# Performance work log

Hardware: AMD Instinct MI355X
Metric: run time of the kernel (lower is better)

Reference implementation:

```python
import jax, jax.numpy as jnp
import numpy as np

EPS = 1e-6

def _layernorm(x, gamma, beta):
    mu = jnp.mean(x, axis=-1, keepdims=True)
    var = jnp.mean(jnp.square(x - mu), axis=-1, keepdims=True)
    return (x - mu) * jax.lax.rsqrt(var + EPS) * gamma + beta


def setup_inputs() -> dict:
    key = jax.random.key(0)
    ks = jax.random.split(key, 8)
    B, N, C, F = 2, 2048, 1024, 4096
    s = 0.02
    return {
        "x": jax.random.normal(ks[0], (B, N, C), jnp.float32),
        "Wq": jax.random.normal(ks[1], (C, C), jnp.float32) * s,
        "Wk": jax.random.normal(ks[2], (C, C), jnp.float32) * s,
        "Wv": jax.random.normal(ks[3], (C, C), jnp.float32) * s,
        "Wp": jax.random.normal(ks[4], (C, C), jnp.float32) * s,
        "bp": jnp.zeros((C,), jnp.float32),
        "W1": jax.random.normal(ks[5], (C, F), jnp.float32) * s,
        "b1": jnp.zeros((F,), jnp.float32),
        "W2": jax.random.normal(ks[6], (F, C), jnp.float32) * s,
        "b2": jnp.zeros((C,), jnp.float32),
        "gamma1": jnp.ones((C,), jnp.float32),
        "beta1": jnp.zeros((C,), jnp.float32),
        "gamma2": jnp.ones((C,), jnp.float32),
        "beta2": jnp.zeros((C,), jnp.float32),
    }


def reference(x, Wq, Wk, Wv, Wp, bp, W1, b1, W2, b2, gamma1, beta1, gamma2, beta2):
    B, N, C = x.shape
    H = 16
    D = C // H
    scale = D ** -0.5

    xn = _layernorm(x, gamma1, beta1)
    # QKV projections (no bias); q pre-scaled by head_dim**-0.5 as in source
    q = (xn @ Wq * scale).reshape(B, N, H, D).transpose(0, 2, 1, 3)  # bhnd
    k = (xn @ Wk).reshape(B, N, H, D).transpose(0, 2, 1, 3)
    v = (xn @ Wv).reshape(B, N, H, D).transpose(0, 2, 1, 3)

    attn = jax.nn.softmax(jnp.einsum("bhnd,bhmd->bhnm", q, k), axis=-1)
    y = jnp.einsum("bhnm,bhmd->bhnd", attn, v)
    y = y.transpose(0, 2, 1, 3).reshape(B, N, C)
    x = x + (y @ Wp + bp)

    xn2 = _layernorm(x, gamma2, beta2)
    h = jax.nn.gelu(xn2 @ W1 + b1, approximate=False)  # keras 'gelu' is exact
    x = x + (h @ W2 + b2)
    return x
```

## Files before the change

kernel.cpp:

```cpp
#include <hip/hip_runtime.h>
#include <math.h>

#define BN  4096
#define SEQ 2048
#define CH  1024
#define FF  4096
#define NH  16
#define HD  64

typedef short bf16x8 __attribute__((ext_vector_type(8)));
typedef float f32x4  __attribute__((ext_vector_type(4)));

#define MFMA16(a,b,c) __builtin_amdgcn_mfma_f32_16x16x32_bf16(a,b,c,0,0,0)

__device__ __forceinline__ unsigned short f2b(float f){
  unsigned u = __float_as_uint(f);
  u += 0x7fffu + ((u>>16)&1u);
  return (unsigned short)(u>>16);
}

__device__ __forceinline__ unsigned pk2(float a, float b){
  return __builtin_amdgcn_perm(__float_as_uint(b), __float_as_uint(a), 0x07060302u);
}

#if __has_builtin(__builtin_amdgcn_exp2f)
__device__ __forceinline__ float fexp2(float x){ return __builtin_amdgcn_exp2f(x); }
#else
__device__ __forceinline__ float fexp2(float x){
  float r; asm("v_exp_f32 %0, %1" : "=v"(r) : "v"(x)); return r;
}
#endif

__device__ __forceinline__ void gl2lds16(const void* g, void* l){
  __builtin_amdgcn_global_load_lds(
      (__attribute__((address_space(1))) void*)g,
      (__attribute__((address_space(3))) void*)l, 16, 0, 0);
}

__device__ __forceinline__ unsigned xcd_chunk(unsigned id, unsigned nwg){
  const unsigned cpx = nwg >> 3;
  return (id & 7u)*cpx + (id >> 3);
}

__global__ __launch_bounds__(256) void transpose_cvt(const float* __restrict__ in,
    unsigned short* __restrict__ out, int R, int S, float scale)
{
  __shared__ float tile[64][65];
  const int tid = threadIdx.x;
  const int tx = tid & 63, ty = tid >> 6;
  const int s0 = blockIdx.x * 64, r0 = blockIdx.y * 64;
  #pragma unroll
  for (int j = 0; j < 16; j++){
    int r = ty + j*4;
    tile[r][tx] = in[(size_t)(r0 + r)*S + s0 + tx];
  }
  __syncthreads();
  #pragma unroll
  for (int j = 0; j < 16; j++){
    int s = ty + j*4;
    out[(size_t)(s0 + s)*R + r0 + tx] = f2b(tile[tx][s] * scale);
  }
}

__global__ __launch_bounds__(256) void ln_kernel(const float* __restrict__ x,
    const float* __restrict__ gamma, const float* __restrict__ beta,
    unsigned short* __restrict__ out)
{
  const int row = blockIdx.x, tid = threadIdx.x;
  const float4 xv = ((const float4*)(x + (size_t)row*CH))[tid];
  float s  = xv.x + xv.y + xv.z + xv.w;
  float ss = xv.x*xv.x + xv.y*xv.y + xv.z*xv.z + xv.w*xv.w;
  #pragma unroll
  for (int off = 1; off < 64; off <<= 1){
    s  += __shfl_xor(s,  off, 64);
    ss += __shfl_xor(ss, off, 64);
  }
  __shared__ float red[8];
  const int w = tid >> 6;
  if ((tid & 63) == 0){ red[w] = s; red[4+w] = ss; }
  __syncthreads();
  s  = red[0]+red[1]+red[2]+red[3];
  ss = red[4]+red[5]+red[6]+red[7];
  const float mu   = s * (1.f/CH);
  const float rstd = rsqrtf(ss*(1.f/CH) - mu*mu + 1e-6f);
  const float4 g = ((const float4*)gamma)[tid];
  const float4 b = ((const float4*)beta )[tid];
  ushort4 o;
  o.x = f2b((xv.x-mu)*rstd*g.x + b.x);
  o.y = f2b((xv.y-mu)*rstd*g.y + b.y);
  o.z = f2b((xv.z-mu)*rstd*g.z + b.z);
  o.w = f2b((xv.w-mu)*rstd*g.w + b.w);
  ((ushort4*)(out + (size_t)row*CH))[tid] = o;
}

template<int BIAS,int GELU,int RES,int OMODE>
__global__ __launch_bounds__(256,4) void gemm128(const unsigned short* __restrict__ A,
    const unsigned short* __restrict__ Bt, const float* __restrict__ bias,
    const float* __restrict__ resid, float* __restrict__ outF,
    unsigned short* __restrict__ outB, unsigned short* __restrict__ outK,
    unsigned short* __restrict__ outV, int M, int Nn, int K)
{
  __shared__ __align__(16) char lds[32768];
  const int tid = threadIdx.x;
  const int w = tid >> 6, lane = tid & 63;
  const int quad = lane >> 4, l16 = lane & 15;
  const unsigned Wid = xcd_chunk(blockIdx.y*gridDim.x + blockIdx.x,
                                 gridDim.x*gridDim.y);
  const int bx = Wid % gridDim.x, by = Wid / gridDim.x;
  const int m0 = by*128, n0 = bx*128;
  const int wm = (w >> 1)*64, wn = (w & 1)*64;
  f32x4 acc[4][4] = {};
  const int nt = K >> 5;

  const int ci0 = w*2, ci1 = w*2 + 1;
  const int ra0 = ci0*16 + (lane >> 2);
  const int ra1 = ra0 + 16;
  const int ga0 = (lane & 3) ^ ((ra0 >> 1) & 3);
  const int ga1 = (lane & 3) ^ ((ra1 >> 1) & 3);
  const unsigned short* aS0 = A  + (size_t)(m0 + ra0)*K + ga0*8;
  const unsigned short* aS1 = A  + (size_t)(m0 + ra1)*K + ga1*8;
  const unsigned short* bS0 = Bt + (size_t)(n0 + ra0)*K + ga0*8;
  const unsigned short* bS1 = Bt + (size_t)(n0 + ra1)*K + ga1*8;

  auto STAGE = [&](int buf){
    char* Ad = lds + buf*8192;
    char* Bd = lds + 16384 + buf*8192;
    gl2lds16(aS0, Ad + ci0*1024);
    gl2lds16(aS1, Ad + ci1*1024);
    gl2lds16(bS0, Bd + ci0*1024);
    gl2lds16(bS1, Bd + ci1*1024);
    aS0 += 32; aS1 += 32; bS0 += 32; bS1 += 32;
  };

  STAGE(0);
  __syncthreads();
  for (int t = 0; t < nt; t++){
    const int cur = t & 1;
    if (t + 1 < nt) STAGE(cur ^ 1);
    const unsigned short* Ac = (const unsigned short*)(lds + cur*8192);
    const unsigned short* Bc = (const unsigned short*)(lds + 16384 + cur*8192);
    bf16x8 af[4], bfr[4];
    #pragma unroll
    for (int mi = 0; mi < 4; mi++){
      const int r = wm + mi*16 + l16;
      af[mi] = *(const bf16x8*)(Ac + r*32 + ((quad ^ ((r >> 1) & 3))*8));
    }
    #pragma unroll
    for (int nj = 0; nj < 4; nj++){
      const int r = wn + nj*16 + l16;
      bfr[nj] = *(const bf16x8*)(Bc + r*32 + ((quad ^ ((r >> 1) & 3))*8));
    }
    #pragma unroll
    for (int mi = 0; mi < 4; mi++)
      #pragma unroll
      for (int nj = 0; nj < 4; nj++)
        acc[mi][nj] = MFMA16(af[mi], bfr[nj], acc[mi][nj]);
    __syncthreads();
  }

  const int colb = n0 + wn;
  const int row0 = m0 + wm;
  if (OMODE == 1 || OMODE == 3){
    unsigned short* scr = (unsigned short*)lds + w*4096;
    const int cg = (OMODE == 3) ? (colb >> 10) : 0;
    #pragma unroll
    for (int nj = 0; nj < 4; nj++){
      const int col = colb + nj*16 + l16;
      const float bv = BIAS ? bias[col] : 0.f;
      #pragma unroll
      for (int mi = 0; mi < 4; mi++){
        #pragma unroll
        for (int r = 0; r < 4; r++){
          const int rl = mi*16 + quad*4 + r;
          float v = acc[mi][nj][r] + bv;
          if (GELU) v = 0.5f*v*(1.f + erff(v*0.70710678118654752f));
          if (RES)  v += resid[(size_t)(row0 + rl)*Nn + col];
          const unsigned short b16 = f2b(v);
          if (OMODE == 3 && cg == 2){
            const int d = nj*16 + l16;
            scr[d*64 + (((rl & 15) << 2) | (rl >> 4))] = b16;
          } else {
            scr[rl*64 + nj*16 + l16] = b16;
          }
        }
      }
    }
    const int sl = (lane & 7)*8;
    #pragma unroll
    for (int j = 0; j < 8; j++){
      const int rr = j*8 + (lane >> 3);
      const bf16x8 vv = *(const bf16x8*)(scr + rr*64 + sl);
      if (OMODE == 1){
        *(bf16x8*)(outB + (size_t)(row0 + rr)*Nn + colb + sl) = vv;
      } else {
        if (cg == 0)
          *(bf16x8*)(outB + (size_t)(row0 + rr)*CH + (colb & (CH-1)) + sl) = vv;
        else if (cg == 1)
          *(bf16x8*)(outK + (size_t)(row0 + rr)*CH + (colb & (CH-1)) + sl) = vv;
        else {
          const int bb = row0 >> 11;
          const int hh = (colb & (CH-1)) >> 6;
          *(bf16x8*)(outV + ((size_t)((bb*NH + hh)*HD) + rr)*SEQ
                          + (row0 & (SEQ-1)) + sl) = vv;
        }
      }
    }
    return;
  }
  #pragma unroll
  for (int nj = 0; nj < 4; nj++){
    const int col = colb + nj*16 + l16;
    const float bv = BIAS ? bias[col] : 0.f;
    #pragma unroll
    for (int mi = 0; mi < 4; mi++){
      #pragma unroll
      for (int r = 0; r < 4; r++){
        const int row = row0 + mi*16 + quad*4 + r;
        float v = acc[mi][nj][r] + bv;
        if (GELU) v = 0.5f*v*(1.f + erff(v*0.70710678118654752f));
        if (RES)  v += resid[(size_t)row*Nn + col];
        outF[(size_t)row*Nn + col] = v;
      }
    }
  }
}

template<int BNT,int BIAS,int GELU,int RES,int OMODE,int SPLITK>
__global__ __launch_bounds__(256,2) void gemm_bt(const unsigned short* __restrict__ A,
    const unsigned short* __restrict__ Bt, const float* __restrict__ bias,
    const float* __restrict__ resid, float* __restrict__ outF,
    unsigned short* __restrict__ outB, unsigned short* __restrict__ outK,
    unsigned short* __restrict__ outV, int M, int Nn, int K)
{
  constexpr int MI  = (BNT==128) ? 4 : 2;
  constexpr int BCH = (BNT==128) ? 4 : 2;
  constexpr int ABYTES = 128*64*2;
  constexpr int BBYTES = BNT*64*2;
  __shared__ __align__(16) char lds[2*ABYTES + 2*BBYTES];
  const int tid = threadIdx.x;
  const int w = tid >> 6, lane = tid & 63;
  const int quad = lane >> 4, l16 = lane & 15;
  const unsigned Wid = xcd_chunk(blockIdx.y*gridDim.x + blockIdx.x,
                                 gridDim.x*gridDim.y);
  const int bx = Wid % gridDim.x, by = Wid / gridDim.x;
  const int m0 = by*128, n0 = bx*BNT;
  const int wm = (BNT==128) ? (w >> 1)*64 : w*32;
  const int wn = (BNT==128) ? (w & 1)*64 : 0;
  const int srow = lane >> 3, sslot = lane & 7;
  f32x4 acc[MI][4] = {};
  const int kseg = SPLITK > 1 ? K / SPLITK : K;
  const int kBeg = SPLITK > 1 ? blockIdx.z * kseg : 0;
  const int nsteps = kseg >> 6;

  auto STAGE = [&](int buf, int k0){
    char* Ad = lds + buf*ABYTES;
    char* Bd = lds + 2*ABYTES + buf*BBYTES;
    #pragma unroll
    for (int i = 0; i < 4; i++){
      const int rb = (w*4 + i)*8;
      const int r = rb + srow;
      const int c = sslot ^ (r & 7);
      gl2lds16(A + (size_t)(m0 + r)*K + k0 + c*8, Ad + rb*128);
    }
    #pragma unroll
    for (int i = 0; i < BCH; i++){
      const int rb = (w*BCH + i)*8;
      const int r = rb + srow;
      const int c = sslot ^ (r & 7);
      gl2lds16(Bt + (size_t)(n0 + r)*K + k0 + c*8, Bd + rb*128);
    }
  };

  STAGE(0, kBeg);
  __syncthreads();
  for (int t = 0; t < nsteps; t++){
    const int cur = t & 1;
    if (t + 1 < nsteps) STAGE(cur ^ 1, kBeg + (t+1)*64);
    const unsigned short* Ac = (const unsigned short*)(lds + cur*ABYTES);
    const unsigned short* Bc = (const unsigned short*)(lds + 2*ABYTES + cur*BBYTES);
    #pragma unroll
    for (int kc = 0; kc < 2; kc++){
      bf16x8 af[MI], bfr[4];
      #pragma unroll
      for (int mi = 0; mi < MI; mi++){
        const int r = wm + mi*16 + l16;
        af[mi] = *(const bf16x8*)(Ac + r*64 + (((kc*4 + quad) ^ (r & 7))*8));
      }
      #pragma unroll
      for (int nj = 0; nj < 4; nj++){
        const int r = wn + nj*16 + l16;
        bfr[nj] = *(const bf16x8*)(Bc + r*64 + (((kc*4 + quad) ^ (r & 7))*8));
      }
      #pragma unroll
      for (int mi = 0; mi < MI; mi++)
        #pragma unroll
        for (int nj = 0; nj < 4; nj++)
          acc[mi][nj] = MFMA16(af[mi], bfr[nj], acc[mi][nj]);
    }
    __syncthreads();
  }

  #pragma unroll
  for (int nj = 0; nj < 4; nj++){
    const int col = n0 + wn + nj*16 + l16;
    const float bv = BIAS ? bias[col] : 0.f;
    #pragma unroll
    for (int mi = 0; mi < MI; mi++){
      #pragma unroll
      for (int r = 0; r < 4; r++){
        const int row = m0 + wm + mi*16 + quad*4 + r;
        float v = acc[mi][nj][r];
        if (SPLITK > 1){
          if (blockIdx.z == 0){
            if (BIAS) v += bias[col];
            if (RES)  v += resid[(size_t)row*Nn + col];
          }
          atomicAdd(&outF[(size_t)row*Nn + col], v);
          continue;
        }
        v += bv;
        if (GELU) v = 0.5f*v*(1.f + erff(v*0.70710678118654752f));
        if (RES)  v += resid[(size_t)row*Nn + col];
        if (OMODE == 0) outF[(size_t)row*Nn + col] = v;
        else outB[(size_t)row*Nn + col] = f2b(v);
      }
    }
  }
}

__global__ __launch_bounds__(256,2) void attn_kernel(const unsigned short* __restrict__ q,
    const unsigned short* __restrict__ k, const unsigned short* __restrict__ vt,
    unsigned short* __restrict__ y)
{
  __shared__ __align__(16) unsigned short Kl[2][64*64];
  __shared__ __align__(16) unsigned short Vl[2][64*64];
  __shared__ __align__(16) unsigned short Pp[4][64*68];
  const int tid = threadIdx.x;
  const int w = tid >> 6, lane = tid & 63;
  const int wq = w & 1, wk = w >> 1;
  const int quad = lane >> 4, l16 = lane & 15;
  const unsigned Wid = xcd_chunk(blockIdx.y*gridDim.x + blockIdx.x,
                                 gridDim.x*gridDim.y);
  const int qt = Wid & 15, bh = Wid >> 4;
  const int b = bh >> 4, h = bh & 15;
  const size_t tb  = ((size_t)b*SEQ)*CH + h*HD;
  const size_t vb_ = (size_t)bh*HD*SEQ;
  const int qr0 = qt*128 + wq*64;

  bf16x8 qf[4][2];
  #pragma unroll
  for (int mi = 0; mi < 4; mi++)
    #pragma unroll
    for (int kc = 0; kc < 2; kc++)
      qf[mi][kc] = *(const bf16x8*)(q + tb + (size_t)(qr0 + mi*16 + l16)*CH + kc*32 + quad*8);

  float sacc[4][4];
  f32x4 o[4][4] = {};
  #pragma unroll
  for (int mi = 0; mi < 4; mi++)
    #pragma unroll
    for (int r = 0; r < 4; r++) sacc[mi][r] = 0.f;

  for (int t = 0; t < 16; t++){
    const int kv0 = wk*1024 + t*64;
    __syncthreads();
    #pragma unroll
    for (int i = 0; i < 8; i++){
      const int r = i*8 + (lane >> 3);
      const int c = (lane & 7) ^ (r & 7);
      if (wq == 0)
        gl2lds16(k  + tb  + (size_t)(kv0 + r)*CH + c*8, (char*)&Kl[wk][0] + i*1024);
      else
        gl2lds16(vt + vb_ + (size_t)r*SEQ + kv0 + c*8, (char*)&Vl[wk][0] + i*1024);
    }
    __syncthreads();

    f32x4 s[4][4] = {};
    #pragma unroll
    for (int kc = 0; kc < 2; kc++){
      #pragma unroll
      for (int nj = 0; nj < 4; nj++){
        bf16x8 kf = *(const bf16x8*)(&Kl[wk][0] + (nj*16 + l16)*64 + (((kc*4 + quad) ^ (l16 & 7))*8));
        #pragma unroll
        for (int mi = 0; mi < 4; mi++)
          s[mi][nj] = MFMA16(qf[mi][kc], kf, s[mi][nj]);
      }
    }
    #pragma unroll
    for (int mi = 0; mi < 4; mi++){
      #pragma unroll
      for (int r = 0; r < 4; r++){
        const float p0 = fexp2(s[mi][0][r]);
        const float p1 = fexp2(s[mi][1][r]);
        const float p2 = fexp2(s[mi][2][r]);
        const float p3 = fexp2(s[mi][3][r]);
        sacc[mi][r] += (p0 + p1) + (p2 + p3);
        uint2 pk;
        pk.x = pk2(p0, p1);
        pk.y = pk2(p2, p3);
        const int prow = mi*16 + quad*4 + r;
        *(uint2*)(&Pp[w][prow*68 + l16*4]) = pk;
      }
    }
    #pragma unroll
    for (int kc = 0; kc < 2; kc++){
      bf16x8 pa[4];
      #pragma unroll
      for (int mi = 0; mi < 4; mi++)
        pa[mi] = *(const bf16x8*)(&Pp[w][(mi*16 + l16)*68 + kc*32 + quad*8]);
      #pragma unroll
      for (int nd = 0; nd < 4; nd++){
        bf16x8 vf = *(const bf16x8*)(&Vl[wk][0] + (nd*16 + l16)*64 + (((kc*4 + quad) ^ (l16 & 7))*8));
        #pragma unroll
        for (int mi = 0; mi < 4; mi++)
          o[mi][nd] = MFMA16(pa[mi], vf, o[mi][nd]);
      }
    }
  }

  __syncthreads();
  float* ob = wq ? (float*)&Vl[0][0] : (float*)&Kl[0][0];
  float* sb = (float*)&Pp[2 + wq][0];
  if (wk == 1){
    #pragma unroll
    for (int mi = 0; mi < 4; mi++)
      #pragma unroll
      for (int nd = 0; nd < 4; nd++)
        #pragma unroll
        for (int r = 0; r < 4; r++){
          const int idx = (mi*4 + nd)*4 + r;
          ob[lane*64 + ((idx + lane) & 63)] = o[mi][nd][r];
        }
    #pragma unroll
    for (int mi = 0; mi < 4; mi++)
      #pragma unroll
      for (int r = 0; r < 4; r++)
        sb[lane*16 + ((mi*4 + r + lane) & 15)] = sacc[mi][r];
  }
  __syncthreads();
  if (wk == 0){
    #pragma unroll
    for (int mi = 0; mi < 4; mi++)
      #pragma unroll
      for (int nd = 0; nd < 4; nd++)
        #pragma unroll
        for (int r = 0; r < 4; r++){
          const int idx = (mi*4 + nd)*4 + r;
          o[mi][nd][r] += ob[lane*64 + ((idx + lane) & 63)];
        }
    #pragma unroll
    for (int mi = 0; mi < 4; mi++){
      #pragma unroll
      for (int r = 0; r < 4; r++){
        float sum = sacc[mi][r] + sb[lane*16 + ((mi*4 + r + lane) & 15)];
        #pragma unroll
        for (int off = 1; off < 16; off <<= 1) sum += __shfl_xor(sum, off, 64);
        const float inv = 1.f / sum;
        const int qr = qr0 + mi*16 + quad*4 + r;
        #pragma unroll
        for (int nd = 0; nd < 4; nd++)
          y[tb + (size_t)qr*CH + nd*16 + l16] = f2b(o[mi][nd][r]*inv);
      }
    }
  }
}

extern "C" void kernel_launch(void* const* d_in, const int* in_sizes, int n_in,
                              void* d_out, int out_size, void* d_ws, size_t ws_size,
                              hipStream_t stream)
{
  (void)in_sizes; (void)n_in; (void)out_size; (void)ws_size;
  const float* x   = (const float*)d_in[0];
  const float* Wq  = (const float*)d_in[1];
  const float* Wk  = (const float*)d_in[2];
  const float* Wv  = (const float*)d_in[3];
  const float* Wp  = (const float*)d_in[4];
  const float* bp  = (const float*)d_in[5];
  const float* W1  = (const float*)d_in[6];
  const float* b1  = (const float*)d_in[7];
  const float* W2  = (const float*)d_in[8];
  const float* b2  = (const float*)d_in[9];
  const float* g1  = (const float*)d_in[10];
  const float* be1 = (const float*)d_in[11];
  const float* g2  = (const float*)d_in[12];
  const float* be2 = (const float*)d_in[13];
  float* out = (float*)d_out;
  char* ws = (char*)d_ws;
  const size_t MB = 1024*1024;
  unsigned short* wq_t = (unsigned short*)(ws +  0*MB);
  unsigned short* wk_t = (unsigned short*)(ws +  2*MB);
  unsigned short* wv_t = (unsigned short*)(ws +  4*MB);
  unsigned short* wp_t = (unsigned short*)(ws +  6*MB);
  unsigned short* w1_t = (unsigned short*)(ws +  8*MB);
  unsigned short* w2_t = (unsigned short*)(ws + 16*MB);
  unsigned short* xn   = (unsigned short*)(ws + 24*MB);
  unsigned short* qb   = (unsigned short*)(ws + 32*MB);
  unsigned short* kb   = (unsigned short*)(ws + 40*MB);
  unsigned short* vtb  = (unsigned short*)(ws + 48*MB);
  unsigned short* yb   = (unsigned short*)(ws + 56*MB);
  float*          x2   = (float*)         (ws + 64*MB);
  unsigned short* xn2  = (unsigned short*)(ws + 80*MB);
  unsigned short* hb   = (unsigned short*)(ws + 88*MB);

  transpose_cvt<<<dim3(16,16),256,0,stream>>>(Wq, wq_t, CH, CH, 0.18033688011112042f);
  transpose_cvt<<<dim3(16,16),256,0,stream>>>(Wk, wk_t, CH, CH, 1.f);
  transpose_cvt<<<dim3(16,16),256,0,stream>>>(Wv, wv_t, CH, CH, 1.f);
  transpose_cvt<<<dim3(16,16),256,0,stream>>>(Wp, wp_t, CH, CH, 1.f);
  transpose_cvt<<<dim3(64,16),256,0,stream>>>(W1, w1_t, CH, FF, 1.f);
  transpose_cvt<<<dim3(16,64),256,0,stream>>>(W2, w2_t, FF, CH, 1.f);

  ln_kernel<<<BN,256,0,stream>>>(x, g1, be1, xn);
  gemm128<0,0,0,3><<<dim3(24,32),256,0,stream>>>(xn, wq_t, nullptr, nullptr,
      nullptr, qb, kb, vtb, BN, 3072, CH);
  attn_kernel<<<dim3(16,32),256,0,stream>>>(qb, kb, vtb, yb);
  gemm_bt<64,1,0,1,0,0><<<dim3(16,32),256,0,stream>>>(yb, wp_t, bp, x, x2,
      nullptr, nullptr, nullptr, BN, CH, CH);
  ln_kernel<<<BN,256,0,stream>>>(x2, g2, be2, xn2);
  gemm128<1,1,0,1><<<dim3(32,32),256,0,stream>>>(xn2, w1_t, b1, nullptr, nullptr,
      hb, nullptr, nullptr, BN, FF, CH);
  gemm_bt<64,1,0,1,0,0><<<dim3(16,32),256,0,stream>>>(hb, w2_t, b2, x2, out,
      nullptr, nullptr, nullptr, BN, CH, FF);
}
```

Measured before the change: 343.7 us.

## Merge weight transposes into one launch, unroll GEMM pipeline, prioritize attention MFMAs

```diff
diff --git a/kernel.cpp b/kernel.cpp
--- a/kernel.cpp
+++ b/kernel.cpp
@@ -42,13 +42,34 @@
   return (id & 7u)*cpx + (id >> 3);
 }
 
-__global__ __launch_bounds__(256) void transpose_cvt(const float* __restrict__ in,
-    unsigned short* __restrict__ out, int R, int S, float scale)
+__global__ __launch_bounds__(256) void transpose_all(
+    const float* __restrict__ Wq, const float* __restrict__ Wk,
+    const float* __restrict__ Wv, const float* __restrict__ Wp,
+    const float* __restrict__ W1, const float* __restrict__ W2,
+    unsigned short* __restrict__ wq_t, unsigned short* __restrict__ wk_t,
+    unsigned short* __restrict__ wv_t, unsigned short* __restrict__ wp_t,
+    unsigned short* __restrict__ w1_t, unsigned short* __restrict__ w2_t)
 {
+  const int id = blockIdx.x;
+  const float* in; unsigned short* out; int R, S, bx, by; float scale = 1.f;
+  if (id < 1024){
+    const int which = id >> 8, t = id & 255;
+    bx = t & 15; by = t >> 4; R = 1024; S = 1024;
+    if (which == 0){ in = Wq; out = wq_t; scale = 0.18033688011112042f; }
+    else if (which == 1){ in = Wk; out = wk_t; }
+    else if (which == 2){ in = Wv; out = wv_t; }
+    else               { in = Wp; out = wp_t; }
+  } else if (id < 2048){
+    const int t = id - 1024; bx = t & 63; by = t >> 6;
+    R = 1024; S = 4096; in = W1; out = w1_t;
+  } else {
+    const int t = id - 2048; bx = t & 15; by = t >> 4;
+    R = 4096; S = 1024; in = W2; out = w2_t;
+  }
   __shared__ float tile[64][65];
   const int tid = threadIdx.x;
   const int tx = tid & 63, ty = tid >> 6;
-  const int s0 = blockIdx.x * 64, r0 = blockIdx.y * 64;
+  const int s0 = bx * 64, r0 = by * 64;
   #pragma unroll
   for (int j = 0; j < 16; j++){
     int r = ty + j*4;
@@ -132,31 +153,50 @@
     aS0 += 32; aS1 += 32; bS0 += 32; bS1 += 32;
   };
 
-  STAGE(0);
-  __syncthreads();
-  for (int t = 0; t < nt; t++){
-    const int cur = t & 1;
-    if (t + 1 < nt) STAGE(cur ^ 1);
-    const unsigned short* Ac = (const unsigned short*)(lds + cur*8192);
-    const unsigned short* Bc = (const unsigned short*)(lds + 16384 + cur*8192);
+  int aoff[4], boff[4];
+  #pragma unroll
+  for (int mi = 0; mi < 4; mi++){
+    const int r = wm + mi*16 + l16;
+    aoff[mi] = r*32 + ((quad ^ ((r >> 1) & 3))*8);
+  }
+  #pragma unroll
+  for (int nj = 0; nj < 4; nj++){
+    const int r = wn + nj*16 + l16;
+    boff[nj] = r*32 + ((quad ^ ((r >> 1) & 3))*8);
+  }
+
+  auto COMPUTE = [&](const unsigned short* Ac, const unsigned short* Bc){
     bf16x8 af[4], bfr[4];
     #pragma unroll
-    for (int mi = 0; mi < 4; mi++){
-      const int r = wm + mi*16 + l16;
-      af[mi] = *(const bf16x8*)(Ac + r*32 + ((quad ^ ((r >> 1) & 3))*8));
-    }
-    #pragma unroll
-    for (int nj = 0; nj < 4; nj++){
-      const int r = wn + nj*16 + l16;
-      bfr[nj] = *(const bf16x8*)(Bc + r*32 + ((quad ^ ((r >> 1) & 3))*8));
-    }
+    for (int mi = 0; mi < 4; mi++) af[mi]  = *(const bf16x8*)(Ac + aoff[mi]);
+    #pragma unroll
+    for (int nj = 0; nj < 4; nj++) bfr[nj] = *(const bf16x8*)(Bc + boff[nj]);
     #pragma unroll
     for (int mi = 0; mi < 4; mi++)
       #pragma unroll
       for (int nj = 0; nj < 4; nj++)
         acc[mi][nj] = MFMA16(af[mi], bfr[nj], acc[mi][nj]);
+  };
+  const unsigned short* A0 = (const unsigned short*)(lds);
+  const unsigned short* A1 = (const unsigned short*)(lds + 8192);
+  const unsigned short* B0 = (const unsigned short*)(lds + 16384);
+  const unsigned short* B1 = (const unsigned short*)(lds + 24576);
+
+  STAGE(0);
+  __syncthreads();
+  for (int t2 = 0; t2 < (nt >> 1) - 1; t2++){
+    STAGE(1);
+    COMPUTE(A0, B0);
     __syncthreads();
-  }
+    STAGE(0);
+    COMPUTE(A1, B1);
+    __syncthreads();
+  }
+  STAGE(1);
+  COMPUTE(A0, B0);
+  __syncthreads();
+  COMPUTE(A1, B1);
+  __syncthreads();
 
   const int colb = n0 + wn;
   const int row0 = m0 + wm;
@@ -376,6 +416,7 @@
     __syncthreads();
 
     f32x4 s[4][4] = {};
+    __builtin_amdgcn_s_setprio(1);
     #pragma unroll
     for (int kc = 0; kc < 2; kc++){
       #pragma unroll
@@ -386,6 +427,7 @@
           s[mi][nj] = MFMA16(qf[mi][kc], kf, s[mi][nj]);
       }
     }
+    __builtin_amdgcn_s_setprio(0);
     #pragma unroll
     for (int mi = 0; mi < 4; mi++){
       #pragma unroll
@@ -402,6 +444,7 @@
         *(uint2*)(&Pp[w][prow*68 + l16*4]) = pk;
       }
     }
+    __builtin_amdgcn_s_setprio(1);
     #pragma unroll
     for (int kc = 0; kc < 2; kc++){
       bf16x8 pa[4];
@@ -416,6 +459,7 @@
           o[mi][nd] = MFMA16(pa[mi], vf, o[mi][nd]);
       }
     }
+    __builtin_amdgcn_s_setprio(0);
   }
 
   __syncthreads();
@@ -502,12 +546,8 @@
   unsigned short* xn2  = (unsigned short*)(ws + 80*MB);
   unsigned short* hb   = (unsigned short*)(ws + 88*MB);
 
-  transpose_cvt<<<dim3(16,16),256,0,stream>>>(Wq, wq_t, CH, CH, 0.18033688011112042f);
-  transpose_cvt<<<dim3(16,16),256,0,stream>>>(Wk, wk_t, CH, CH, 1.f);
-  transpose_cvt<<<dim3(16,16),256,0,stream>>>(Wv, wv_t, CH, CH, 1.f);
-  transpose_cvt<<<dim3(16,16),256,0,stream>>>(Wp, wp_t, CH, CH, 1.f);
-  transpose_cvt<<<dim3(64,16),256,0,stream>>>(W1, w1_t, CH, FF, 1.f);
-  transpose_cvt<<<dim3(16,64),256,0,stream>>>(W2, w2_t, FF, CH, 1.f);
+  transpose_all<<<dim3(3072),256,0,stream>>>(Wq, Wk, Wv, Wp, W1, W2,
+      wq_t, wk_t, wv_t, wp_t, w1_t, w2_t);
 
   ln_kernel<<<BN,256,0,stream>>>(x, g1, be1, xn);
   gemm128<0,0,0,3><<<dim3(24,32),256,0,stream>>>(xn, wq_t, nullptr, nullptr,
```

New measurement: 325.3 us. 5.4% less time.
